# Kernel tuning notes

Hardware: AMD Instinct MI355X
Metric: run time of the kernel (lower is better)

## Reference

```python
import jax, jax.numpy as jnp
import numpy as np

S, P, C, H, K = 16, 512, 768, 12, 6
D = C // H


def setup_inputs() -> dict:
    key = jax.random.key(0)
    k0, k1, k2 = jax.random.split(key, 3)
    x = jax.random.normal(k0, (1, S * P, C), jnp.float32)
    Wqkv = jax.random.normal(k1, (C, 3 * C), jnp.float32) * (C ** -0.5)
    bqkv = jnp.zeros((3 * C,), jnp.float32)
    Wproj = jax.random.normal(k2, (C, C), jnp.float32) * (C ** -0.5)
    bproj = jnp.zeros((C,), jnp.float32)
    # each frame i is covisible with K frames (itself + K-1 temporal neighbours)
    covis_idx = jnp.asarray((np.arange(S)[:, None] + np.arange(K)[None, :]) % S,
                            jnp.int32)  # [S, K]
    return {"x": x, "Wqkv": Wqkv, "bqkv": bqkv,
            "Wproj": Wproj, "bproj": bproj, "covis_idx": covis_idx}


def reference(x, Wqkv, bqkv, Wproj, bproj, covis_idx):
    B, N, C_ = x.shape
    S_, K_ = covis_idx.shape
    P_ = N // S_
    # qkv projection -> [3, B, H, N, D]
    qkv = (x @ Wqkv + bqkv).reshape(B, N, 3, H, D).transpose(2, 0, 3, 1, 4)
    q, k, v = qkv[0], qkv[1], qkv[2]
    kf = k.reshape(B, H, S_, P_, D)          # keys grouped by frame
    vf = v.reshape(B, H, S_, P_, D)
    qf = q.reshape(B, H, S_, P_, D).transpose(2, 0, 1, 3, 4)  # [S,B,H,P,D]
    scale = jnp.float32(D) ** -0.5

    def step(_, inp):
        q_i, idx = inp                        # q_i [B,H,P,D], idx [K]
        k_c = kf[:, :, idx].reshape(B, H, K_ * P_, D)   # gather covisible tokens
        v_c = vf[:, :, idx].reshape(B, H, K_ * P_, D)
        s = jnp.einsum('bhpd,bhnd->bhpn', q_i, k_c) * scale
        a = jax.nn.softmax(s, axis=-1)
        return None, jnp.einsum('bhpn,bhnd->bhpd', a, v_c)

    _, out = jax.lax.scan(step, None, (qf, covis_idx))  # [S,B,H,P,D]
    out = out.transpose(1, 0, 3, 2, 4).reshape(B, N, C_)  # [B, S*P, H*D]
    return out @ Wproj + bproj
```

## Files before the change

kernel.cpp:

```cpp
#include <hip/hip_runtime.h>
#include <stdint.h>

typedef __bf16 bf16;
typedef __bf16 bf16x4 __attribute__((ext_vector_type(4)));
typedef __bf16 bf16x8 __attribute__((ext_vector_type(8)));
typedef float floatx4 __attribute__((ext_vector_type(4)));
typedef short short4v __attribute__((ext_vector_type(4)));

#define NTOK 8192
#define HEADSZ 524288L

#if defined(__has_builtin)
#if __has_builtin(__builtin_amdgcn_mfma_f32_16x16x16bf16_1k)
#define HAVE_MFMA16_BUILTIN 1
#endif
#endif
__device__ __forceinline__ floatx4 mfma16(short4v a, short4v b, floatx4 c) {
#ifdef HAVE_MFMA16_BUILTIN
  return __builtin_amdgcn_mfma_f32_16x16x16bf16_1k(a, b, c, 0, 0, 0);
#else
  floatx4 d;
  asm("v_mfma_f32_16x16x16_bf16 %0, %1, %2, %3" : "=v"(d) : "v"(a), "v"(b), "v"(c));
  return d;
#endif
}

__device__ __forceinline__ void gload16(const bf16* g, bf16* l) {
  __builtin_amdgcn_global_load_lds(
      (const __attribute__((address_space(1))) uint8_t*)g,
      (__attribute__((address_space(3))) uint8_t*)l, 16, 0, 0);
}

__global__ void detect_kernel(const unsigned short* __restrict__ x, int* __restrict__ flag) {
  int lane = threadIdx.x & 63;
  int cnt = 0;
#pragma unroll
  for (int i = 0; i < 4; ++i) {
    unsigned int u = x[2 * (lane * 4 + i)];
    float v = __uint_as_float(u << 16);
    if (!(fabsf(v) <= 1e4f)) cnt++;
  }
#pragma unroll
  for (int off = 1; off < 64; off <<= 1) cnt += __shfl_xor(cnt, off, 64);
  if (threadIdx.x == 0) *flag = (cnt > 32) ? 1 : 0;
}

__global__ __launch_bounds__(256) void ingest_kernel(
    const void* s0, const void* s1, const void* s2,
    bf16* d0, bf16* d1, bf16* d2, const int* __restrict__ flag) {
  const long b0 = 6291456, b1 = b0 + 2304, b2 = b1 + 768;
  long g = ((long)blockIdx.x * 256 + threadIdx.x) * 8;
  if (g >= b2) return;
  const void* src; bf16* dst; long off;
  if (g < b0)      { src = s0; dst = d0; off = g; }
  else if (g < b1) { src = s1; dst = d1; off = g - b0; }
  else             { src = s2; dst = d2; off = g - b1; }
  if (*flag) {
    const float* s = (const float*)src + off;
#pragma unroll
    for (int e = 0; e < 8; ++e) dst[off + e] = (bf16)s[e];
  } else {
    *(uint4*)(dst + off) = *(const uint4*)((const bf16*)src + off);
  }
}

__global__ __launch_bounds__(256) void transposeW_kernel(
    const void* __restrict__ in, bf16* __restrict__ out, int R, int Ccols,
    const int* __restrict__ flag) {
  __shared__ bf16 t[32][33];
  int bx = blockIdx.x * 32, by = blockIdx.y * 32;
  int tx = threadIdx.x & 31, ty = threadIdx.x >> 5;
  const bool f32 = (*flag != 0);
#pragma unroll
  for (int i = ty; i < 32; i += 8) {
    long src = (long)(by + i) * Ccols + bx + tx;
    t[i][tx] = f32 ? (bf16)((const float*)in)[src] : ((const bf16*)in)[src];
  }
  __syncthreads();
#pragma unroll
  for (int i = ty; i < 32; i += 8) out[(long)(bx + i) * R + by + tx] = t[tx][i];
}

template <int EPI>
__global__ __launch_bounds__(256, 2) void gemm_kernel(
    const bf16* __restrict__ A, const bf16* __restrict__ BT,
    const bf16* __restrict__ bias, void* __restrict__ Cout,
    int M, int N, int Kd, const int* __restrict__ flag) {
  __shared__ bf16 As[128 * 32];
  __shared__ bf16 Bs[128 * 32];
  const int tid = threadIdx.x;
  const int w = tid >> 6, lane = tid & 63;
  const int quad = lane >> 4, l15 = lane & 15;
  const int m0 = blockIdx.x * 128, n0 = blockIdx.y * 128;
  const int wm = w >> 1, wn = w & 1;
  const int srow = lane >> 2;
  const int scol = (lane & 3) * 8;

  floatx4 acc[4][4] = {};
  const bf16* ga = A + (long)(m0 + 32 * w + srow) * Kd + scol;
  const bf16* gb = BT + (long)(n0 + 32 * w + srow) * Kd + scol;
  bf16* la = As + 32 * w * 32;
  bf16* lb = Bs + 32 * w * 32;

  for (int kk = 0; kk < Kd; kk += 32) {
    __syncthreads();
    gload16(ga + kk, la);
    gload16(ga + kk + 16 * Kd, la + 16 * 32);
    gload16(gb + kk, lb);
    gload16(gb + kk + 16 * Kd, lb + 16 * 32);
    __syncthreads();
    bf16x8 fa[4], fb[4];
#pragma unroll
    for (int i = 0; i < 4; ++i)
      fa[i] = *(const bf16x8*)(As + (64 * wm + 16 * i + l15) * 32 + quad * 8);
#pragma unroll
    for (int j = 0; j < 4; ++j)
      fb[j] = *(const bf16x8*)(Bs + (64 * wn + 16 * j + l15) * 32 + quad * 8);
#pragma unroll
    for (int i = 0; i < 4; ++i)
#pragma unroll
      for (int j = 0; j < 4; ++j)
        acc[i][j] = __builtin_amdgcn_mfma_f32_16x16x32_bf16(fa[i], fb[j], acc[i][j], 0, 0, 0);
  }

  const bool outf32 = (EPI == 0) && (flag[0] != 0);
#pragma unroll
  for (int i = 0; i < 4; ++i) {
#pragma unroll
    for (int j = 0; j < 4; ++j) {
      const int col = n0 + 64 * wn + 16 * j + l15;
      const float bv = (float)bias[col];
#pragma unroll
      for (int r = 0; r < 4; ++r) {
        const int row = m0 + 64 * wm + 16 * i + quad * 4 + r;
        float v = acc[i][j][r] + bv;
        if (EPI == 1) {
          const int which = col / 768;
          if (which == 0) v *= 0.18033688011112042f;
          const int rem = col - which * 768;
          const int hh = rem >> 6, d = rem & 63;
          const long base = ((long)which * 12 + hh) * HEADSZ + (long)(row >> 6) * 4096;
          long off;
          if (which < 2)
            off = base + (d >> 3) * 512 + (row & 63) * 8 + (d & 7);
          else
            off = base + ((row & 63) >> 3) * 512 + d * 8 + (row & 7);
          ((bf16*)Cout)[off] = (bf16)v;
        } else {
          if (outf32) ((float*)Cout)[(long)row * N + col] = v;
          else        ((bf16*)Cout)[(long)row * N + col] = (bf16)v;
        }
      }
    }
  }
}

__global__ __launch_bounds__(256, 2) void attn_kernel(
    const bf16* __restrict__ qkv, const int* __restrict__ covis,
    bf16* __restrict__ attnout) {
  __shared__ bf16 db[2][16384];

  const int tid = threadIdx.x;
  const int w = tid >> 6, lane = tid & 63;
  const int quad = lane >> 4, l15 = lane & 15;
  const int sb = w >> 1, hf = w & 1;

  const int xcd = blockIdx.x & 7;
  const int idx = blockIdx.x >> 3;
  const int qt = idx & 7;
  const int fh = xcd * 24 + (idx >> 3);
  const int h = fh >> 4, f = fh & 15;
  const int qtb = f * 8 + qt;

  const bf16* qb = qkv + (long)(0 * 12 + h) * HEADSZ;
  const bf16* kb = qkv + (long)(1 * 12 + h) * HEADSZ;
  const bf16* vb = qkv + (long)(2 * 12 + h) * HEADSZ;

  int frames[6];
#pragma unroll
  for (int j = 0; j < 6; ++j) frames[j] = covis[f * 6 + j];

  bf16x8 qa[2][4];
  {
    const bf16* qblk = qb + (long)qtb * 4096;
#pragma unroll
    for (int s = 0; s < 2; ++s)
#pragma unroll
      for (int nt = 0; nt < 4; ++nt)
        qa[s][nt] = *(const bf16x8*)(qblk + (4 * s + quad) * 512 + (nt * 16 + l15) * 8);
  }

  bf16x4 ones4;
#pragma unroll
  for (int e = 0; e < 4; ++e) ones4[e] = (bf16)1.0f;
  const short4v onesv = __builtin_bit_cast(short4v, ones4);

  floatx4 o[16] = {};
  floatx4 osum[4] = {};

  const int krow = 32 * hf + l15;

  auto issue = [&](int c) {
    const int tb0 = frames[c >> 2] * 8 + (c & 3) * 2;
    bf16* base = db[c & 1];
    const bf16* kg = kb + (long)tb0 * 4096 + w * 2048;
    const bf16* vg = vb + (long)tb0 * 4096 + w * 2048;
#pragma unroll
    for (int i = 0; i < 4; ++i) gload16(kg + i * 512 + lane * 8, base + w * 2048 + i * 512);
#pragma unroll
    for (int i = 0; i < 4; ++i) gload16(vg + i * 512 + lane * 8, base + 8192 + w * 2048 + i * 512);
  };

  issue(0);
  for (int c = 0; c < 24; ++c) {
    __syncthreads();
    if (c < 23) issue(c + 1);
    const bf16* Ks = db[c & 1];
    const bf16* Vs = db[c & 1] + 8192;

#pragma unroll
    for (int mt = 0; mt < 2; ++mt) {
      floatx4 st[4] = {};
#pragma unroll
      for (int s = 0; s < 2; ++s) {
        bf16x8 kf = *(const bf16x8*)(Ks + ((sb * 8 + 4 * s + quad) * 64 + krow + 16 * mt) * 8);
#pragma unroll
        for (int nt = 0; nt < 4; ++nt)
          st[nt] = __builtin_amdgcn_mfma_f32_16x16x32_bf16(kf, qa[s][nt], st[nt], 0, 0, 0);
      }
      short4v p[4];
#pragma unroll
      for (int nt = 0; nt < 4; ++nt) {
        bf16x4 pb;
#pragma unroll
        for (int r = 0; r < 4; ++r) pb[r] = (bf16)__builtin_amdgcn_exp2f(st[nt][r]);
        p[nt] = __builtin_bit_cast(short4v, pb);
      }
#pragma unroll
      for (int nt = 0; nt < 4; ++nt) osum[nt] = mfma16(onesv, p[nt], osum[nt]);
#pragma unroll
      for (int mtd = 0; mtd < 4; ++mtd) {
        bf16x4 vf = *(const bf16x4*)(Vs + ((sb * 8 + 4 * hf + 2 * mt + (quad >> 1)) * 64 +
                                           mtd * 16 + l15) * 8 + (quad & 1) * 4);
        short4v va = __builtin_bit_cast(short4v, vf);
#pragma unroll
        for (int nt = 0; nt < 4; ++nt)
          o[mtd * 4 + nt] = mfma16(va, p[nt], o[mtd * 4 + nt]);
      }
    }
  }

  __syncthreads();
  float* sc = (float*)db[1];
#pragma unroll
  for (int nt = 0; nt < 4; ++nt) sc[(w * 4 + nt) * 64 + lane] = osum[nt][0];
  __syncthreads();
  float inv[4];
#pragma unroll
  for (int nt = 0; nt < 4; ++nt) {
    float tot = sc[nt * 64 + lane] + sc[(4 + nt) * 64 + lane] +
                sc[(8 + nt) * 64 + lane] + sc[(12 + nt) * 64 + lane];
    inv[nt] = 1.0f / tot;
  }
  __syncthreads();

  float* buf0 = (float*)db[0];
  float* buf1 = (float*)(db[0] + 8192);
  if (w == 2) {
#pragma unroll
    for (int t = 0; t < 16; ++t) *(floatx4*)(buf0 + (t * 64 + lane) * 4) = o[t];
  } else if (w == 3) {
#pragma unroll
    for (int t = 0; t < 16; ++t) *(floatx4*)(buf1 + (t * 64 + lane) * 4) = o[t];
  }
  __syncthreads();
  if (w == 0) {
#pragma unroll
    for (int t = 0; t < 16; ++t) o[t] += *(const floatx4*)(buf0 + (t * 64 + lane) * 4);
  } else if (w == 1) {
#pragma unroll
    for (int t = 0; t < 16; ++t) o[t] += *(const floatx4*)(buf1 + (t * 64 + lane) * 4);
  }
  __syncthreads();
  if (w == 1) {
#pragma unroll
    for (int t = 0; t < 16; ++t) *(floatx4*)(buf0 + (t * 64 + lane) * 4) = o[t];
  }
  __syncthreads();
  if (w == 0) {
    bf16* ob = (bf16*)db[1];
#pragma unroll
    for (int mtd = 0; mtd < 4; ++mtd)
#pragma unroll
      for (int nt = 0; nt < 4; ++nt) {
        floatx4 t = o[mtd * 4 + nt] + *(const floatx4*)(buf0 + ((mtd * 4 + nt) * 64 + lane) * 4);
        bf16x4 bv;
#pragma unroll
        for (int r = 0; r < 4; ++r) bv[r] = (bf16)(t[r] * inv[nt]);
        *(bf16x4*)(ob + (nt * 16 + l15) * 64 + mtd * 16 + quad * 4) = bv;
      }
    bf16* dst = attnout + ((long)qtb * 64 + lane) * 768 + h * 64;
#pragma unroll
    for (int i = 0; i < 8; ++i)
      *(bf16x8*)(dst + i * 8) = *(const bf16x8*)(ob + lane * 64 + i * 8);
  }
}

extern "C" void kernel_launch(void* const* d_in, const int* in_sizes, int n_in,
                              void* d_out, int out_size, void* d_ws, size_t ws_size,
                              hipStream_t stream) {
  const void* x     = d_in[0];
  const void* Wqkv  = d_in[1];
  const void* bqkv  = d_in[2];
  const void* Wproj = d_in[3];
  const void* bproj = d_in[4];
  const int*  covis = (const int*)d_in[5];

  char* ws = (char*)d_ws;
  size_t off = 0;
  auto alloc = [&](size_t bytes) {
    char* p = ws + off;
    off += (bytes + 255) & ~(size_t)255;
    return p;
  };
  int*  flag   = (int*)alloc(256);
  bf16* xc     = (bf16*)alloc(6291456UL * 2);
  bf16* bqkvc  = (bf16*)alloc(2304UL * 2);
  bf16* bprojc = (bf16*)alloc(768UL * 2);
  bf16* WqkvT  = (bf16*)alloc(1769472UL * 2);
  bf16* WprojT = (bf16*)alloc(589824UL * 2);
  bf16* qkvws  = (bf16*)alloc(3UL * 12 * 8192 * 64 * 2);
  bf16* attnw  = (bf16*)alloc(6291456UL * 2);

  detect_kernel<<<1, 64, 0, stream>>>((const unsigned short*)x, flag);
  ingest_kernel<<<3074, 256, 0, stream>>>(x, bqkv, bproj, xc, bqkvc, bprojc, flag);
  transposeW_kernel<<<dim3(72, 24), 256, 0, stream>>>(Wqkv, WqkvT, 768, 2304, flag);
  transposeW_kernel<<<dim3(24, 24), 256, 0, stream>>>(Wproj, WprojT, 768, 768, flag);
  gemm_kernel<1><<<dim3(64, 18), 256, 0, stream>>>(xc, WqkvT, bqkvc, qkvws, 8192, 2304, 768, flag);
  attn_kernel<<<1536, 256, 0, stream>>>(qkvws, covis, attnw);
  gemm_kernel<0><<<dim3(64, 6), 256, 0, stream>>>(attnw, WprojT, bprojc, d_out, 8192, 768, 768, flag);
}
```

Baseline: 278.0 us.

## Share K/V tiles across four query tiles per block and vectorize GEMM epilogue stores

The attention kernel now runs 512-thread blocks that process four query tiles from the same frame and head. Each staged K/V chunk is therefore reused by four query tiles, which cuts global K/V traffic by four times. Row sums are now accumulated in registers with shuffles instead of ones-vector MFMAs, and the cross-wave output reduction is simplified to a two-way split. The GEMM swaps MFMA operand order for Q/K and plain outputs so each lane holds four consecutive columns, which enables 4-wide vector stores in the epilogue. Risks include lower block count (384 blocks), higher register pressure under launch_bounds(512,4), and LDS-sharing limits on occupancy.

```diff
diff --git a/kernel.cpp b/kernel.cpp
--- a/kernel.cpp
+++ b/kernel.cpp
@@ -7,7 +7,6 @@
 typedef float floatx4 __attribute__((ext_vector_type(4)));
 typedef short short4v __attribute__((ext_vector_type(4)));
 
-#define NTOK 8192
 #define HEADSZ 524288L
 
 #if defined(__has_builtin)
@@ -96,6 +95,9 @@
   const int srow = lane >> 2;
   const int scol = (lane & 3) * 8;
 
+  const int which = (EPI == 1) ? (n0 / 768) : 0;
+  const bool tr = (EPI == 0) || (which < 2);
+
   floatx4 acc[4][4] = {};
   const bf16* ga = A + (long)(m0 + 32 * w + srow) * Kd + scol;
   const bf16* gb = BT + (long)(n0 + 32 * w + srow) * Kd + scol;
@@ -116,46 +118,79 @@
 #pragma unroll
     for (int j = 0; j < 4; ++j)
       fb[j] = *(const bf16x8*)(Bs + (64 * wn + 16 * j + l15) * 32 + quad * 8);
-#pragma unroll
-    for (int i = 0; i < 4; ++i)
-#pragma unroll
-      for (int j = 0; j < 4; ++j)
-        acc[i][j] = __builtin_amdgcn_mfma_f32_16x16x32_bf16(fa[i], fb[j], acc[i][j], 0, 0, 0);
+    if (tr) {
+#pragma unroll
+      for (int i = 0; i < 4; ++i)
+#pragma unroll
+        for (int j = 0; j < 4; ++j)
+          acc[i][j] = __builtin_amdgcn_mfma_f32_16x16x32_bf16(fb[j], fa[i], acc[i][j], 0, 0, 0);
+    } else {
+#pragma unroll
+      for (int i = 0; i < 4; ++i)
+#pragma unroll
+        for (int j = 0; j < 4; ++j)
+          acc[i][j] = __builtin_amdgcn_mfma_f32_16x16x32_bf16(fa[i], fb[j], acc[i][j], 0, 0, 0);
+    }
   }
 
   const bool outf32 = (EPI == 0) && (flag[0] != 0);
-#pragma unroll
-  for (int i = 0; i < 4; ++i) {
-#pragma unroll
-    for (int j = 0; j < 4; ++j) {
-      const int col = n0 + 64 * wn + 16 * j + l15;
-      const float bv = (float)bias[col];
-#pragma unroll
-      for (int r = 0; r < 4; ++r) {
-        const int row = m0 + 64 * wm + 16 * i + quad * 4 + r;
-        float v = acc[i][j][r] + bv;
+  if (tr) {
+#pragma unroll
+    for (int i = 0; i < 4; ++i) {
+      const int row = m0 + 64 * wm + 16 * i + l15;
+#pragma unroll
+      for (int j = 0; j < 4; ++j) {
+        const int col0 = n0 + 64 * wn + 16 * j + quad * 4;
+        floatx4 v = acc[i][j];
+#pragma unroll
+        for (int r = 0; r < 4; ++r) v[r] += (float)bias[col0 + r];
         if (EPI == 1) {
-          const int which = col / 768;
-          if (which == 0) v *= 0.18033688011112042f;
-          const int rem = col - which * 768;
-          const int hh = rem >> 6, d = rem & 63;
-          const long base = ((long)which * 12 + hh) * HEADSZ + (long)(row >> 6) * 4096;
-          long off;
-          if (which < 2)
-            off = base + (d >> 3) * 512 + (row & 63) * 8 + (d & 7);
-          else
-            off = base + ((row & 63) >> 3) * 512 + d * 8 + (row & 7);
-          ((bf16*)Cout)[off] = (bf16)v;
+          if (which == 0) {
+#pragma unroll
+            for (int r = 0; r < 4; ++r) v[r] *= 0.18033688011112042f;
+          }
+          const int rem = col0 - which * 768;
+          const int hh = rem >> 6, d0 = rem & 63;
+          const long off = ((long)which * 12 + hh) * HEADSZ + (long)(row >> 6) * 4096 +
+                           (d0 >> 3) * 512 + (row & 63) * 8 + (d0 & 7);
+          bf16x4 bv;
+#pragma unroll
+          for (int r = 0; r < 4; ++r) bv[r] = (bf16)v[r];
+          *(bf16x4*)((bf16*)Cout + off) = bv;
         } else {
-          if (outf32) ((float*)Cout)[(long)row * N + col] = v;
-          else        ((bf16*)Cout)[(long)row * N + col] = (bf16)v;
+          if (outf32) {
+            *(floatx4*)((float*)Cout + (long)row * N + col0) = v;
+          } else {
+            bf16x4 bv;
+#pragma unroll
+            for (int r = 0; r < 4; ++r) bv[r] = (bf16)v[r];
+            *(bf16x4*)((bf16*)Cout + (long)row * N + col0) = bv;
+          }
         }
       }
     }
-  }
-}
-
-__global__ __launch_bounds__(256, 2) void attn_kernel(
+  } else {
+#pragma unroll
+    for (int i = 0; i < 4; ++i) {
+      const int row0 = m0 + 64 * wm + 16 * i + quad * 4;
+#pragma unroll
+      for (int j = 0; j < 4; ++j) {
+        const int col = n0 + 64 * wn + 16 * j + l15;
+        const float bv = (float)bias[col];
+        const int rem = col - 2 * 768;
+        const int hh = rem >> 6, d = rem & 63;
+        const long off = ((long)2 * 12 + hh) * HEADSZ + (long)(row0 >> 6) * 4096 +
+                         ((row0 & 63) >> 3) * 512 + d * 8 + (row0 & 7);
+        bf16x4 ov;
+#pragma unroll
+        for (int r = 0; r < 4; ++r) ov[r] = (bf16)(acc[i][j][r] + bv);
+        *(bf16x4*)((bf16*)Cout + off) = ov;
+      }
+    }
+  }
+}
+
+__global__ __launch_bounds__(512, 4) void attn_kernel(
     const bf16* __restrict__ qkv, const int* __restrict__ covis,
     bf16* __restrict__ attnout) {
   __shared__ bf16 db[2][16384];
@@ -163,14 +198,14 @@
   const int tid = threadIdx.x;
   const int w = tid >> 6, lane = tid & 63;
   const int quad = lane >> 4, l15 = lane & 15;
-  const int sb = w >> 1, hf = w & 1;
+  const int g = w >> 1, kh = w & 1;
 
   const int xcd = blockIdx.x & 7;
   const int idx = blockIdx.x >> 3;
-  const int qt = idx & 7;
-  const int fh = xcd * 24 + (idx >> 3);
+  const int qhalf = idx & 1;
+  const int fh = xcd * 24 + (idx >> 1);
   const int h = fh >> 4, f = fh & 15;
-  const int qtb = f * 8 + qt;
+  const int qtb = f * 8 + qhalf * 4 + g;
 
   const bf16* qb = qkv + (long)(0 * 12 + h) * HEADSZ;
   const bf16* kb = qkv + (long)(1 * 12 + h) * HEADSZ;
@@ -190,40 +225,30 @@
         qa[s][nt] = *(const bf16x8*)(qblk + (4 * s + quad) * 512 + (nt * 16 + l15) * 8);
   }
 
-  bf16x4 ones4;
-#pragma unroll
-  for (int e = 0; e < 4; ++e) ones4[e] = (bf16)1.0f;
-  const short4v onesv = __builtin_bit_cast(short4v, ones4);
-
   floatx4 o[16] = {};
-  floatx4 osum[4] = {};
-
-  const int krow = 32 * hf + l15;
+  float rsum[4] = {0.f, 0.f, 0.f, 0.f};
 
   auto issue = [&](int c) {
     const int tb0 = frames[c >> 2] * 8 + (c & 3) * 2;
-    bf16* base = db[c & 1];
-    const bf16* kg = kb + (long)tb0 * 4096 + w * 2048;
-    const bf16* vg = vb + (long)tb0 * 4096 + w * 2048;
-#pragma unroll
-    for (int i = 0; i < 4; ++i) gload16(kg + i * 512 + lane * 8, base + w * 2048 + i * 512);
-#pragma unroll
-    for (int i = 0; i < 4; ++i) gload16(vg + i * 512 + lane * 8, base + 8192 + w * 2048 + i * 512);
+    const bf16* src = (w < 4 ? kb : vb) + (long)tb0 * 4096 + (w & 3) * 2048;
+    bf16* dst = db[c & 1] + (w >= 4 ? 8192 : 0) + (w & 3) * 2048;
+#pragma unroll
+    for (int i = 0; i < 4; ++i) gload16(src + i * 512 + lane * 8, dst + i * 512);
   };
 
   issue(0);
   for (int c = 0; c < 24; ++c) {
     __syncthreads();
     if (c < 23) issue(c + 1);
-    const bf16* Ks = db[c & 1];
-    const bf16* Vs = db[c & 1] + 8192;
-
-#pragma unroll
-    for (int mt = 0; mt < 2; ++mt) {
+    const bf16* Kb = db[c & 1] + kh * 4096;
+    const bf16* Vb = db[c & 1] + 8192 + kh * 4096;
+
+#pragma unroll
+    for (int mt = 0; mt < 4; ++mt) {
       floatx4 st[4] = {};
 #pragma unroll
       for (int s = 0; s < 2; ++s) {
-        bf16x8 kf = *(const bf16x8*)(Ks + ((sb * 8 + 4 * s + quad) * 64 + krow + 16 * mt) * 8);
+        bf16x8 kf = *(const bf16x8*)(Kb + ((4 * s + quad) * 64 + mt * 16 + l15) * 8);
 #pragma unroll
         for (int nt = 0; nt < 4; ++nt)
           st[nt] = __builtin_amdgcn_mfma_f32_16x16x32_bf16(kf, qa[s][nt], st[nt], 0, 0, 0);
@@ -233,15 +258,17 @@
       for (int nt = 0; nt < 4; ++nt) {
         bf16x4 pb;
 #pragma unroll
-        for (int r = 0; r < 4; ++r) pb[r] = (bf16)__builtin_amdgcn_exp2f(st[nt][r]);
+        for (int r = 0; r < 4; ++r) {
+          float e = __builtin_amdgcn_exp2f(st[nt][r]);
+          pb[r] = (bf16)e;
+          rsum[nt] += e;
+        }
         p[nt] = __builtin_bit_cast(short4v, pb);
       }
 #pragma unroll
-      for (int nt = 0; nt < 4; ++nt) osum[nt] = mfma16(onesv, p[nt], osum[nt]);
-#pragma unroll
       for (int mtd = 0; mtd < 4; ++mtd) {
-        bf16x4 vf = *(const bf16x4*)(Vs + ((sb * 8 + 4 * hf + 2 * mt + (quad >> 1)) * 64 +
-                                           mtd * 16 + l15) * 8 + (quad & 1) * 4);
+        bf16x4 vf = *(const bf16x4*)(Vb + ((2 * mt + (quad >> 1)) * 64 + mtd * 16 + l15) * 8 +
+                                     (quad & 1) * 4);
         short4v va = __builtin_bit_cast(short4v, vf);
 #pragma unroll
         for (int nt = 0; nt < 4; ++nt)
@@ -251,58 +278,43 @@
   }
 
   __syncthreads();
-  float* sc = (float*)db[1];
-#pragma unroll
-  for (int nt = 0; nt < 4; ++nt) sc[(w * 4 + nt) * 64 + lane] = osum[nt][0];
+#pragma unroll
+  for (int nt = 0; nt < 4; ++nt) {
+    rsum[nt] += __shfl_xor(rsum[nt], 16, 64);
+    rsum[nt] += __shfl_xor(rsum[nt], 32, 64);
+  }
+  float* sums = (float*)(&db[0][0]);
+  if (quad == 0) {
+#pragma unroll
+    for (int nt = 0; nt < 4; ++nt) sums[((g * 2 + kh) * 4 + nt) * 16 + l15] = rsum[nt];
+  }
   __syncthreads();
   float inv[4];
 #pragma unroll
-  for (int nt = 0; nt < 4; ++nt) {
-    float tot = sc[nt * 64 + lane] + sc[(4 + nt) * 64 + lane] +
-                sc[(8 + nt) * 64 + lane] + sc[(12 + nt) * 64 + lane];
-    inv[nt] = 1.0f / tot;
-  }
-  __syncthreads();
-
-  float* buf0 = (float*)db[0];
-  float* buf1 = (float*)(db[0] + 8192);
-  if (w == 2) {
-#pragma unroll
-    for (int t = 0; t < 16; ++t) *(floatx4*)(buf0 + (t * 64 + lane) * 4) = o[t];
-  } else if (w == 3) {
-#pragma unroll
-    for (int t = 0; t < 16; ++t) *(floatx4*)(buf1 + (t * 64 + lane) * 4) = o[t];
-  }
-  __syncthreads();
-  if (w == 0) {
-#pragma unroll
-    for (int t = 0; t < 16; ++t) o[t] += *(const floatx4*)(buf0 + (t * 64 + lane) * 4);
-  } else if (w == 1) {
-#pragma unroll
-    for (int t = 0; t < 16; ++t) o[t] += *(const floatx4*)(buf1 + (t * 64 + lane) * 4);
-  }
-  __syncthreads();
-  if (w == 1) {
-#pragma unroll
-    for (int t = 0; t < 16; ++t) *(floatx4*)(buf0 + (t * 64 + lane) * 4) = o[t];
-  }
-  __syncthreads();
-  if (w == 0) {
-    bf16* ob = (bf16*)db[1];
-#pragma unroll
-    for (int mtd = 0; mtd < 4; ++mtd)
+  for (int nt = 0; nt < 4; ++nt)
+    inv[nt] = 1.0f / (rsum[nt] + sums[((g * 2 + (1 - kh)) * 4 + nt) * 16 + l15]);
+  __syncthreads();
+
+  float* scr = (float*)(&db[0][0]);
+  if (kh == 1) {
+#pragma unroll
+    for (int t = 0; t < 16; ++t) *(floatx4*)(scr + g * 4096 + (t * 64 + lane) * 4) = o[t];
+  }
+  __syncthreads();
+  if (kh == 0) {
+#pragma unroll
+    for (int mtd = 0; mtd < 4; ++mtd) {
 #pragma unroll
       for (int nt = 0; nt < 4; ++nt) {
-        floatx4 t = o[mtd * 4 + nt] + *(const floatx4*)(buf0 + ((mtd * 4 + nt) * 64 + lane) * 4);
+        const int t = mtd * 4 + nt;
+        floatx4 v = o[t] + *(const floatx4*)(scr + g * 4096 + (t * 64 + lane) * 4);
         bf16x4 bv;
 #pragma unroll
-        for (int r = 0; r < 4; ++r) bv[r] = (bf16)(t[r] * inv[nt]);
-        *(bf16x4*)(ob + (nt * 16 + l15) * 64 + mtd * 16 + quad * 4) = bv;
-      }
-    bf16* dst = attnout + ((long)qtb * 64 + lane) * 768 + h * 64;
-#pragma unroll
-    for (int i = 0; i < 8; ++i)
-      *(bf16x8*)(dst + i * 8) = *(const bf16x8*)(ob + lane * 64 + i * 8);
+        for (int r = 0; r < 4; ++r) bv[r] = (bf16)(v[r] * inv[nt]);
+        const long token = (long)qtb * 64 + nt * 16 + l15;
+        *(bf16x4*)(attnout + token * 768 + h * 64 + mtd * 16 + quad * 4) = bv;
+      }
+    }
   }
 }
 
@@ -337,6 +349,6 @@
   transposeW_kernel<<<dim3(72, 24), 256, 0, stream>>>(Wqkv, WqkvT, 768, 2304, flag);
   transposeW_kernel<<<dim3(24, 24), 256, 0, stream>>>(Wproj, WprojT, 768, 768, flag);
   gemm_kernel<1><<<dim3(64, 18), 256, 0, stream>>>(xc, WqkvT, bqkvc, qkvws, 8192, 2304, 768, flag);
-  attn_kernel<<<1536, 256, 0, stream>>>(qkvws, covis, attnw);
+  attn_kernel<<<384, 512, 0, stream>>>(qkvws, covis, attnw);
   gemm_kernel<0><<<dim3(64, 6), 256, 0, stream>>>(attnw, WprojT, bprojc, d_out, 8192, 768, 768, flag);
 }
```

Result: slower. 893.8 us (+221.5%).
